# Kernel optimization log

Measured on AMD Instinct MI355X. Metric: run time of the kernel, lower is better.

Reference implementation:

```python
import jax, jax.numpy as jnp
import numpy as np

MODEL_DIM = 1024
NUM_HEADS = 16
HEAD_DIM = MODEL_DIM // NUM_HEADS
EPS = 1e-12
CHUNK = 128  # chunk size for the linear-attention recurrence


def setup_inputs() -> dict:
    key = jax.random.key(0)
    kx, kq, kk, kv, ko = jax.random.split(key, 5)
    b, l = 4, 4096
    x = jax.random.normal(kx, (b, l, MODEL_DIM), dtype=jnp.float32)
    # nn.Linear weights, init std=0.02, no bias; torch Linear computes x @ W.T
    Wq = 0.02 * jax.random.normal(kq, (MODEL_DIM, MODEL_DIM), dtype=jnp.float32)
    Wk = 0.02 * jax.random.normal(kk, (MODEL_DIM, MODEL_DIM), dtype=jnp.float32)
    Wv = 0.02 * jax.random.normal(kv, (MODEL_DIM, MODEL_DIM), dtype=jnp.float32)
    Wo = 0.02 * jax.random.normal(ko, (MODEL_DIM, MODEL_DIM), dtype=jnp.float32)
    return {"x": x, "Wq": Wq, "Wk": Wk, "Wv": Wv, "Wo": Wo}


def _pos_elu(t):
    # feature_map = F.elu(x) + 1
    return jax.nn.elu(t) + 1.0


def _linear_attention(q, k, v):
    # q,k,v: (b,h,l,d) with feature map already applied.
    # Causal linear attention: out_t = (q_t . sum_{s<=t} k_s v_s^T) / (q_t . sum_{s<=t} k_s) + EPS
    # Chunked recurrence over the (d,d) KV state avoids the (b,h,l,d,d) cumsum.
    b, h, l, d = q.shape
    nc = l // CHUNK
    qc = jnp.moveaxis(q.reshape(b, h, nc, CHUNK, d), 2, 0)  # (nc,b,h,C,d)
    kc = jnp.moveaxis(k.reshape(b, h, nc, CHUNK, d), 2, 0)
    vc = jnp.moveaxis(v.reshape(b, h, nc, CHUNK, d), 2, 0)
    mask = jnp.tril(jnp.ones((CHUNK, CHUNK), dtype=q.dtype))  # causal within chunk

    def step(carry, inp):
        S, z = carry  # S:(b,h,d,d) running sum k v^T; z:(b,h,d) running sum k
        qb, kb, vb = inp  # (b,h,C,d)
        scores = jnp.einsum('bhcd,bhsd->bhcs', qb, kb) * mask  # (b,h,C,C)
        num = jnp.einsum('bhcd,bhde->bhce', qb, S) + jnp.einsum('bhcs,bhse->bhce', scores, vb)
        den = jnp.einsum('bhcd,bhd->bhc', qb, z) + scores.sum(-1)  # (b,h,C)
        out = num / den[..., None] + EPS  # NOTE: eps added after division, as in source
        S = S + jnp.einsum('bhsd,bhse->bhde', kb, vb)
        z = z + kb.sum(axis=2)
        return (S, z), out

    S0 = jnp.zeros((b, h, d, d), dtype=q.dtype)
    z0 = jnp.zeros((b, h, d), dtype=q.dtype)
    _, outs = jax.lax.scan(step, (S0, z0), (qc, kc, vc))  # (nc,b,h,C,d)
    # -> (b, l, h, d)
    return jnp.moveaxis(outs, 0, 1).transpose(0, 3, 1, 2, 4).reshape(b, h * 0 + l // l, 0, 0) if False else outs


def reference(x, Wq, Wk, Wv, Wo):
    b, l, D = x.shape
    h, d = NUM_HEADS, HEAD_DIM
    # projections (torch Linear: x @ W.T), split heads -> (b,h,l,d)
    q = (x @ Wq.T).reshape(b, l, h, d).transpose(0, 2, 1, 3)
    k = (x @ Wk.T).reshape(b, l, h, d).transpose(0, 2, 1, 3)
    v = (x @ Wv.T).reshape(b, l, h, d).transpose(0, 2, 1, 3)
    q = _pos_elu(q)
    k = _pos_elu(k)
    outs = _linear_attention(q, k, v)  # (nc,b,h,C,d)
    nc = l // CHUNK
    # (nc,b,h,C,d) -> (b,nc,C,h,d) -> (b,l,D)  (matches transpose(1,2).view in torch)
    attn = outs.transpose(1, 0, 3, 2, 4).reshape(b, l, D)
    return attn @ Wo.T
```

## Files before the change

kernel.cpp:

```cpp
#include <hip/hip_runtime.h>
#include <stdint.h>

typedef float f32x4 __attribute__((ext_vector_type(4)));
typedef __bf16 bf16x8 __attribute__((ext_vector_type(8)));
typedef unsigned short u16x8 __attribute__((ext_vector_type(8)));

#define DEV __device__ __forceinline__

DEV unsigned short f2bf(float f) {
  unsigned int u = __float_as_uint(f);
  unsigned int r = (u + 0x7FFFu + ((u >> 16) & 1u)) >> 16;
  return (unsigned short)r;
}
DEV float b2f(unsigned short h) { return __uint_as_float(((unsigned int)h) << 16); }

DEV void gload16(const void* g, void* l) {
  __builtin_amdgcn_global_load_lds((__attribute__((address_space(1))) void*)(g),
                                   (__attribute__((address_space(3))) void*)(l), 16, 0, 0);
}

__global__ void cast_bf16_kernel(const float* __restrict__ in,
                                 unsigned short* __restrict__ out, int n8) {
  int i = blockIdx.x * 256 + threadIdx.x;
  if (i >= n8) return;
  const float4* p = (const float4*)in + (size_t)i * 2;
  float4 a = p[0], b = p[1];
  u16x8 o;
  o[0] = f2bf(a.x); o[1] = f2bf(a.y); o[2] = f2bf(a.z); o[3] = f2bf(a.w);
  o[4] = f2bf(b.x); o[5] = f2bf(b.y); o[6] = f2bf(b.z); o[7] = f2bf(b.w);
  ((u16x8*)out)[i] = o;
}

__global__ void cast_w4(const float* __restrict__ Wq, const float* __restrict__ Wk,
                        const float* __restrict__ Wv, const float* __restrict__ Wo,
                        unsigned short* __restrict__ wqkv, unsigned short* __restrict__ wo) {
  int i = blockIdx.x * 256 + threadIdx.x;
  int sel = i >> 17, j = i & 131071;
  const float* src = (sel == 0) ? Wq : (sel == 1) ? Wk : (sel == 2) ? Wv : Wo;
  unsigned short* dst = (sel < 3) ? (wqkv + (size_t)sel * 1048576) : wo;
  const float4* p = (const float4*)src + (size_t)j * 2;
  float4 a = p[0], b = p[1];
  u16x8 o;
  o[0] = f2bf(a.x); o[1] = f2bf(a.y); o[2] = f2bf(a.z); o[3] = f2bf(a.w);
  o[4] = f2bf(b.x); o[5] = f2bf(b.y); o[6] = f2bf(b.z); o[7] = f2bf(b.w);
  ((u16x8*)dst)[j] = o;
}

template<int MODE>
__global__ __launch_bounds__(256, 2) void gemm_bt(
    const unsigned short* __restrict__ A, const unsigned short* __restrict__ Bw,
    void* __restrict__ out0, unsigned short* __restrict__ qp,
    unsigned short* __restrict__ kp, unsigned short* __restrict__ vp,
    int K, int N, int nTn)
{
  __shared__ unsigned short sA[128 * 64];
  __shared__ unsigned short sB[128 * 64];
  int t = threadIdx.x, w = t >> 6, lane = t & 63, fr = lane & 15, fq = lane >> 4;
  int nwg = gridDim.x, cpx = nwg >> 3;
  int bid = (blockIdx.x & 7) * cpx + (blockIdx.x >> 3);
  int bm = bid / nTn, bn = bid % nTn;
  int wm = w >> 1, wn = w & 1;

  f32x4 acc[4][4];
  f32x4 z4 = {0.f, 0.f, 0.f, 0.f};
#pragma unroll
  for (int mi = 0; mi < 4; ++mi)
#pragma unroll
    for (int ni = 0; ni < 4; ++ni) acc[mi][ni] = z4;

  for (int k0 = 0; k0 < K; k0 += 64) {
#pragma unroll
    for (int i = 0; i < 4; ++i) {
      int p = (i * 4 + w) * 64 + lane;
      int r = p >> 3;
      int c8 = (p & 7) ^ (r & 7);
      gload16(A + (size_t)(bm * 128 + r) * K + k0 + c8 * 8, &sA[(i * 4 + w) * 512]);
      gload16(Bw + (size_t)(bn * 128 + r) * K + k0 + c8 * 8, &sB[(i * 4 + w) * 512]);
    }
    __syncthreads();
#pragma unroll
    for (int ks = 0; ks < 2; ++ks) {
      bf16x8 af[4], bg[4];
#pragma unroll
      for (int mi = 0; mi < 4; ++mi) {
        int r = wm * 64 + mi * 16 + fr;
        int c8 = (ks * 4 + fq) ^ (r & 7);
        af[mi] = *(const bf16x8*)&sA[(r * 8 + c8) * 8];
      }
#pragma unroll
      for (int ni = 0; ni < 4; ++ni) {
        int r = wn * 64 + ni * 16 + fr;
        int c8 = (ks * 4 + fq) ^ (r & 7);
        bg[ni] = *(const bf16x8*)&sB[(r * 8 + c8) * 8];
      }
#pragma unroll
      for (int mi = 0; mi < 4; ++mi)
#pragma unroll
        for (int ni = 0; ni < 4; ++ni)
          acc[mi][ni] = __builtin_amdgcn_mfma_f32_16x16x32_bf16(af[mi], bg[ni], acc[mi][ni], 0, 0, 0);
    }
    __syncthreads();
  }

  if (MODE == 0) {
    float* O = (float*)out0;
#pragma unroll
    for (int mi = 0; mi < 4; ++mi)
#pragma unroll
      for (int ni = 0; ni < 4; ++ni)
#pragma unroll
        for (int j = 0; j < 4; ++j) {
          int m = bm * 128 + wm * 64 + mi * 16 + fq * 4 + j;
          int n = bn * 128 + wn * 64 + ni * 16 + fr;
          O[(size_t)m * N + n] = acc[mi][ni][j];
        }
  } else {
    int tsel = (bn * 128) >> 10;
    unsigned short* base = (tsel == 0) ? qp : ((tsel == 1) ? kp : vp);
#pragma unroll
    for (int mi = 0; mi < 4; ++mi)
#pragma unroll
      for (int ni = 0; ni < 4; ++ni)
#pragma unroll
        for (int j = 0; j < 4; ++j) {
          int m = bm * 128 + wm * 64 + mi * 16 + fq * 4 + j;
          int n = bn * 128 + wn * 64 + ni * 16 + fr;
          int col1 = n & 1023;
          int h = col1 >> 6, d = col1 & 63;
          int b = m >> 12, l = m & 4095;
          float v = acc[mi][ni][j];
          if (tsel < 2) v = (v > 0.f) ? (v + 1.f) : __expf(v);
          base[(((size_t)(b * 16 + h)) * 4096 + l) * 64 + d] = f2bf(v);
        }
  }
}

__global__ __launch_bounds__(256) void chunk_state(
    const unsigned short* __restrict__ kb, const unsigned short* __restrict__ vb,
    float* __restrict__ Sbuf, float* __restrict__ zbuf)
{
  __shared__ unsigned short kT[64 * 136];
  __shared__ unsigned short vT[64 * 136];
  int t = threadIdx.x, w = t >> 6, lane = t & 63, fr = lane & 15, fq = lane >> 4;
  int bh = blockIdx.x >> 5, c = blockIdx.x & 31;
  size_t base = ((size_t)bh * 4096 + (size_t)c * 128) * 64;

  int s = t >> 1, d0 = (t & 1) * 32;
  const unsigned short* kpp = kb + base + (size_t)s * 64 + d0;
  const unsigned short* vpp = vb + base + (size_t)s * 64 + d0;
#pragma unroll
  for (int i = 0; i < 4; ++i) {
    u16x8 kr = *(const u16x8*)(kpp + i * 8);
    u16x8 vr = *(const u16x8*)(vpp + i * 8);
#pragma unroll
    for (int j = 0; j < 8; ++j) {
      int d = d0 + i * 8 + j;
      kT[d * 136 + s] = kr[j];
      vT[d * 136 + s] = vr[j];
    }
  }
  __syncthreads();

  f32x4 acc[4];
  f32x4 z4 = {0.f, 0.f, 0.f, 0.f};
#pragma unroll
  for (int n = 0; n < 4; ++n) acc[n] = z4;
#pragma unroll
  for (int ks = 0; ks < 4; ++ks) {
    bf16x8 av = *(const bf16x8*)&vT[(w * 16 + fr) * 136 + ks * 32 + fq * 8];
#pragma unroll
    for (int n = 0; n < 4; ++n) {
      bf16x8 bk = *(const bf16x8*)&kT[(n * 16 + fr) * 136 + ks * 32 + fq * 8];
      acc[n] = __builtin_amdgcn_mfma_f32_16x16x32_bf16(av, bk, acc[n], 0, 0, 0);
    }
  }
  size_t ob = ((size_t)bh * 32 + c) * 4096;
#pragma unroll
  for (int n = 0; n < 4; ++n)
#pragma unroll
    for (int j = 0; j < 4; ++j) {
      int e = w * 16 + fq * 4 + j, d = n * 16 + fr;
      Sbuf[ob + (size_t)e * 64 + d] = acc[n][j];
    }
  if (t < 64) {
    float z = 0.f;
#pragma unroll
    for (int i = 0; i < 16; ++i) {
      u16x8 kr = *(const u16x8*)&kT[t * 136 + i * 8];
#pragma unroll
      for (int j = 0; j < 8; ++j) z += b2f(kr[j]);
    }
    zbuf[((size_t)bh * 32 + c) * 64 + t] = z;
  }
}

__global__ __launch_bounds__(256) void scan_S(
    const float* __restrict__ Sbuf, unsigned short* __restrict__ Spref)
{
  int idx = blockIdx.x * 256 + threadIdx.x;
  int bh = idx >> 12, i = idx & 4095;
  size_t base = (size_t)bh * 32 * 4096 + i;
  float run = 0.f;
#pragma unroll
  for (int c = 0; c < 32; ++c) {
    float v = Sbuf[base + (size_t)c * 4096];
    Spref[base + (size_t)c * 4096] = f2bf(run);
    run += v;
  }
}

__global__ __launch_bounds__(256) void scan_z(
    const float* __restrict__ zbuf, float* __restrict__ zpref)
{
  int idx = blockIdx.x * 256 + threadIdx.x;
  size_t base = (size_t)(idx >> 6) * 32 * 64 + (idx & 63);
  float run = 0.f;
#pragma unroll
  for (int c = 0; c < 32; ++c) {
    float v = zbuf[base + c * 64];
    zpref[base + c * 64] = run;
    run += v;
  }
}

__global__ __launch_bounds__(256, 2) void chunk_out(
    const unsigned short* __restrict__ qb, const unsigned short* __restrict__ kb,
    const unsigned short* __restrict__ vb, const unsigned short* __restrict__ Spref,
    const float* __restrict__ zpref, unsigned short* __restrict__ attn)
{
  __shared__ unsigned short sq[128 * 64];
  __shared__ unsigned short skv[128 * 64];
  __shared__ unsigned short ss[128 * 128];
  __shared__ unsigned short sS[80 * 64];
  int t = threadIdx.x, w = t >> 6, lane = t & 63, fr = lane & 15, fq = lane >> 4;
  int bh = blockIdx.x >> 5, c = blockIdx.x & 31;
  size_t qkbase = ((size_t)bh * 4096 + (size_t)c * 128) * 64;
  size_t sbase = ((size_t)bh * 32 + c) * 4096;

  u16x8 vreg[4];
#pragma unroll
  for (int i = 0; i < 4; ++i)
    vreg[i] = *(const u16x8*)(vb + qkbase + (size_t)(t * 4 + i) * 8);

#pragma unroll
  for (int i = 0; i < 4; ++i) {
    int p = t * 4 + i, r = p >> 3, c8 = p & 7;
    int sw = (r * 8 + (c8 ^ (r & 7))) * 8;
    *(u16x8*)&sq[sw] = *(const u16x8*)(qb + qkbase + (size_t)p * 8);
    *(u16x8*)&skv[sw] = *(const u16x8*)(kb + qkbase + (size_t)p * 8);
  }
#pragma unroll
  for (int i = 0; i < 2; ++i) {
    int p = t * 2 + i, e = p >> 3, c8 = p & 7;
    *(u16x8*)&sS[(e * 8 + (c8 ^ (e & 7))) * 8] = *(const u16x8*)(Spref + sbase + (size_t)p * 8);
  }
  if (t < 64) sS[64 * 64 + t] = f2bf(zpref[((size_t)bh * 32 + c) * 64 + t]);
  {
    unsigned int* zz = (unsigned int*)&sS[65 * 64];
    for (int i = t; i < 480; i += 256) zz[i] = 0u;
  }
  __syncthreads();

  int rowbase = w * 32;
  bf16x8 aq[2][2];
#pragma unroll
  for (int mi = 0; mi < 2; ++mi)
#pragma unroll
    for (int kt = 0; kt < 2; ++kt) {
      int r = rowbase + mi * 16 + fr;
      int c8 = (kt * 4 + fq) ^ (r & 7);
      aq[mi][kt] = *(const bf16x8*)&sq[(r * 8 + c8) * 8];
    }

  f32x4 accs[2][8];
  f32x4 z4 = {0.f, 0.f, 0.f, 0.f};
#pragma unroll
  for (int mi = 0; mi < 2; ++mi)
#pragma unroll
    for (int ni = 0; ni < 8; ++ni) accs[mi][ni] = z4;

#pragma unroll
  for (int ni = 0; ni < 8; ++ni)
#pragma unroll
    for (int kt = 0; kt < 2; ++kt) {
      int r = ni * 16 + fr;
      int c8 = (kt * 4 + fq) ^ (r & 7);
      bf16x8 bk = *(const bf16x8*)&skv[(r * 8 + c8) * 8];
      accs[0][ni] = __builtin_amdgcn_mfma_f32_16x16x32_bf16(aq[0][kt], bk, accs[0][ni], 0, 0, 0);
      accs[1][ni] = __builtin_amdgcn_mfma_f32_16x16x32_bf16(aq[1][kt], bk, accs[1][ni], 0, 0, 0);
    }

  float rs[2][4];
#pragma unroll
  for (int mi = 0; mi < 2; ++mi)
#pragma unroll
    for (int j = 0; j < 4; ++j) {
      int srow = rowbase + mi * 16 + fq * 4 + j;
      float sum = 0.f;
#pragma unroll
      for (int ni = 0; ni < 8; ++ni) {
        int scol = ni * 16 + fr;
        float v = accs[mi][ni][j];
        v = (scol <= srow) ? v : 0.f;
        accs[mi][ni][j] = v;
        sum += v;
      }
#pragma unroll
      for (int msk = 1; msk < 16; msk <<= 1) sum += __shfl_xor(sum, msk, 64);
      rs[mi][j] = sum;
    }
  __syncthreads();

#pragma unroll
  for (int i = 0; i < 4; ++i) {
    int p = t * 4 + i, s = p >> 3, e0g = (p & 7) * 8;
#pragma unroll
    for (int j = 0; j < 8; ++j) {
      int e = e0g + j;
      skv[(e * 16 + ((s >> 3) ^ (e & 15))) * 8 + (s & 7)] = vreg[i][j];
    }
  }
#pragma unroll
  for (int mi = 0; mi < 2; ++mi)
#pragma unroll
    for (int ni = 0; ni < 8; ++ni)
#pragma unroll
      for (int j = 0; j < 4; ++j) {
        int srow = rowbase + mi * 16 + fq * 4 + j;
        int scol = ni * 16 + fr;
        ss[(srow * 16 + ((scol >> 3) ^ (srow & 15))) * 8 + (scol & 7)] = f2bf(accs[mi][ni][j]);
      }
  __syncthreads();

  f32x4 acco[2][4];
  f32x4 accd[2];
#pragma unroll
  for (int mi = 0; mi < 2; ++mi) {
    accd[mi] = z4;
#pragma unroll
    for (int ni = 0; ni < 4; ++ni) acco[mi][ni] = z4;
  }
#pragma unroll
  for (int kt = 0; kt < 2; ++kt) {
#pragma unroll
    for (int ni = 0; ni < 4; ++ni) {
      int r = ni * 16 + fr;
      int c8 = (kt * 4 + fq) ^ (r & 7);
      bf16x8 bS = *(const bf16x8*)&sS[(r * 8 + c8) * 8];
      acco[0][ni] = __builtin_amdgcn_mfma_f32_16x16x32_bf16(aq[0][kt], bS, acco[0][ni], 0, 0, 0);
      acco[1][ni] = __builtin_amdgcn_mfma_f32_16x16x32_bf16(aq[1][kt], bS, acco[1][ni], 0, 0, 0);
    }
    {
      int r = 64 + fr;
      int c8 = (kt * 4 + fq) ^ (r & 7);
      bf16x8 bz = *(const bf16x8*)&sS[(r * 8 + c8) * 8];
      accd[0] = __builtin_amdgcn_mfma_f32_16x16x32_bf16(aq[0][kt], bz, accd[0], 0, 0, 0);
      accd[1] = __builtin_amdgcn_mfma_f32_16x16x32_bf16(aq[1][kt], bz, accd[1], 0, 0, 0);
    }
  }
#pragma unroll
  for (int kt = 0; kt < 4; ++kt) {
    bf16x8 am[2];
#pragma unroll
    for (int mi = 0; mi < 2; ++mi) {
      int r = rowbase + mi * 16 + fr;
      int c8 = (kt * 4 + fq) ^ (r & 15);
      am[mi] = *(const bf16x8*)&ss[(r * 16 + c8) * 8];
    }
#pragma unroll
    for (int ni = 0; ni < 4; ++ni) {
      int r = ni * 16 + fr;
      int c8 = (kt * 4 + fq) ^ (r & 15);
      bf16x8 bv = *(const bf16x8*)&skv[(r * 16 + c8) * 8];
      acco[0][ni] = __builtin_amdgcn_mfma_f32_16x16x32_bf16(am[0], bv, acco[0][ni], 0, 0, 0);
      acco[1][ni] = __builtin_amdgcn_mfma_f32_16x16x32_bf16(am[1], bv, acco[1][ni], 0, 0, 0);
    }
  }

  int b = bh >> 4, h = bh & 15;
#pragma unroll
  for (int mi = 0; mi < 2; ++mi)
#pragma unroll
    for (int j = 0; j < 4; ++j) {
      float den = __shfl(accd[mi][j], (lane & 48), 64) + rs[mi][j];
      float rden = 1.f / den;
      int m = rowbase + mi * 16 + fq * 4 + j;
      size_t rowoff = ((size_t)b * 4096 + (size_t)c * 128 + m) * 1024 + h * 64;
#pragma unroll
      for (int ni = 0; ni < 4; ++ni) {
        int e = ni * 16 + fr;
        float o = acco[mi][ni][j] * rden + 1e-12f;
        attn[rowoff + e] = f2bf(o);
      }
    }
}

extern "C" void kernel_launch(void* const* d_in, const int* in_sizes, int n_in,
                              void* d_out, int out_size, void* d_ws, size_t ws_size,
                              hipStream_t stream) {
  (void)in_sizes; (void)n_in; (void)out_size; (void)ws_size;
  const float* x = (const float*)d_in[0];
  const float* Wq = (const float*)d_in[1];
  const float* Wk = (const float*)d_in[2];
  const float* Wv = (const float*)d_in[3];
  const float* Wo = (const float*)d_in[4];
  char* ws = (char*)d_ws;
  unsigned short* xbf  = (unsigned short*)(ws + 0);
  unsigned short* wqkv = (unsigned short*)(ws + 33554432);
  unsigned short* wo   = (unsigned short*)(ws + 39845888);
  unsigned short* q    = (unsigned short*)(ws + 41943040);
  unsigned short* k    = (unsigned short*)(ws + 75497472);
  unsigned short* v    = (unsigned short*)(ws + 109051904);
  unsigned short* attn = (unsigned short*)(ws + 142606336);
  float* Sbuf          = (float*)(ws + 176160768);
  unsigned short* Spref= (unsigned short*)(ws + 209715200);
  float* zbuf          = (float*)(ws + 226492416);
  float* zpref         = (float*)(ws + 227016704);

  cast_bf16_kernel<<<8192, 256, 0, stream>>>(x, xbf, 2097152);
  cast_w4<<<2048, 256, 0, stream>>>(Wq, Wk, Wv, Wo, wqkv, wo);

  gemm_bt<1><<<3072, 256, 0, stream>>>(xbf, wqkv, nullptr, q, k, v, 1024, 3072, 24);
  chunk_state<<<2048, 256, 0, stream>>>(k, v, Sbuf, zbuf);
  scan_S<<<1024, 256, 0, stream>>>(Sbuf, Spref);
  scan_z<<<16, 256, 0, stream>>>(zbuf, zpref);
  chunk_out<<<2048, 256, 0, stream>>>(q, k, v, Spref, zpref, attn);
  gemm_bt<0><<<1024, 256, 0, stream>>>(attn, wo, d_out, nullptr, nullptr, nullptr, 1024, 1024, 8);
}
```

Before: 234.8 us.

## Fuse x bf16 cast into QKV GEMM, merge scan kernels, drop block swizzle

Removes the standalone fp32->bf16 cast of x: the QKV GEMM now loads fp32 x through registers, converts it, and writes it to swizzled LDS, while B still uses direct global-to-LDS loads. The two prefix-scan kernels are merged into one launch, and the XCD-aware block remapping in the GEMM is replaced by plain blockIdx ordering. This saves a 64MB round trip and a kernel launch, but the A tile is now read at twice the bytes per GEMM tile with register staging and no async LDS path, which may stall the GEMM main loop. Dropping the swizzle may also hurt L2 locality across XCDs.

```diff
diff --git a/kernel.cpp b/kernel.cpp
--- a/kernel.cpp
+++ b/kernel.cpp
@@ -17,18 +17,6 @@
 DEV void gload16(const void* g, void* l) {
   __builtin_amdgcn_global_load_lds((__attribute__((address_space(1))) void*)(g),
                                    (__attribute__((address_space(3))) void*)(l), 16, 0, 0);
-}
-
-__global__ void cast_bf16_kernel(const float* __restrict__ in,
-                                 unsigned short* __restrict__ out, int n8) {
-  int i = blockIdx.x * 256 + threadIdx.x;
-  if (i >= n8) return;
-  const float4* p = (const float4*)in + (size_t)i * 2;
-  float4 a = p[0], b = p[1];
-  u16x8 o;
-  o[0] = f2bf(a.x); o[1] = f2bf(a.y); o[2] = f2bf(a.z); o[3] = f2bf(a.w);
-  o[4] = f2bf(b.x); o[5] = f2bf(b.y); o[6] = f2bf(b.z); o[7] = f2bf(b.w);
-  ((u16x8*)out)[i] = o;
 }
 
 __global__ void cast_w4(const float* __restrict__ Wq, const float* __restrict__ Wk,
@@ -48,7 +36,7 @@
 
 template<int MODE>
 __global__ __launch_bounds__(256, 2) void gemm_bt(
-    const unsigned short* __restrict__ A, const unsigned short* __restrict__ Bw,
+    const void* __restrict__ Aptr, const unsigned short* __restrict__ Bw,
     void* __restrict__ out0, unsigned short* __restrict__ qp,
     unsigned short* __restrict__ kp, unsigned short* __restrict__ vp,
     int K, int N, int nTn)
@@ -56,8 +44,7 @@
   __shared__ unsigned short sA[128 * 64];
   __shared__ unsigned short sB[128 * 64];
   int t = threadIdx.x, w = t >> 6, lane = t & 63, fr = lane & 15, fq = lane >> 4;
-  int nwg = gridDim.x, cpx = nwg >> 3;
-  int bid = (blockIdx.x & 7) * cpx + (blockIdx.x >> 3);
+  int bid = blockIdx.x;
   int bm = bid / nTn, bn = bid % nTn;
   int wm = w >> 1, wn = w & 1;
 
@@ -69,13 +56,45 @@
     for (int ni = 0; ni < 4; ++ni) acc[mi][ni] = z4;
 
   for (int k0 = 0; k0 < K; k0 += 64) {
-#pragma unroll
-    for (int i = 0; i < 4; ++i) {
-      int p = (i * 4 + w) * 64 + lane;
-      int r = p >> 3;
-      int c8 = (p & 7) ^ (r & 7);
-      gload16(A + (size_t)(bm * 128 + r) * K + k0 + c8 * 8, &sA[(i * 4 + w) * 512]);
-      gload16(Bw + (size_t)(bn * 128 + r) * K + k0 + c8 * 8, &sB[(i * 4 + w) * 512]);
+    if (MODE == 1) {
+      const float* A32 = (const float*)Aptr;
+#pragma unroll
+      for (int i = 0; i < 4; ++i) {
+        int p = (i * 4 + w) * 64 + lane;
+        int r = p >> 3;
+        int c8 = (p & 7) ^ (r & 7);
+        gload16(Bw + (size_t)(bn * 128 + r) * K + k0 + c8 * 8, &sB[(i * 4 + w) * 512]);
+      }
+      float4 av[4][2];
+#pragma unroll
+      for (int i = 0; i < 4; ++i) {
+        int p = (i * 4 + w) * 64 + lane;
+        int r = p >> 3, c8 = p & 7;
+        const float* s = A32 + (size_t)(bm * 128 + r) * K + k0 + c8 * 8;
+        av[i][0] = *(const float4*)s;
+        av[i][1] = *(const float4*)(s + 4);
+      }
+#pragma unroll
+      for (int i = 0; i < 4; ++i) {
+        int p = (i * 4 + w) * 64 + lane;
+        int r = p >> 3, c8 = p & 7;
+        u16x8 o;
+        o[0] = f2bf(av[i][0].x); o[1] = f2bf(av[i][0].y);
+        o[2] = f2bf(av[i][0].z); o[3] = f2bf(av[i][0].w);
+        o[4] = f2bf(av[i][1].x); o[5] = f2bf(av[i][1].y);
+        o[6] = f2bf(av[i][1].z); o[7] = f2bf(av[i][1].w);
+        *(u16x8*)&sA[(r * 8 + (c8 ^ (r & 7))) * 8] = o;
+      }
+    } else {
+      const unsigned short* A16 = (const unsigned short*)Aptr;
+#pragma unroll
+      for (int i = 0; i < 4; ++i) {
+        int p = (i * 4 + w) * 64 + lane;
+        int r = p >> 3;
+        int c8 = (p & 7) ^ (r & 7);
+        gload16(A16 + (size_t)(bm * 128 + r) * K + k0 + c8 * 8, &sA[(i * 4 + w) * 512]);
+        gload16(Bw + (size_t)(bn * 128 + r) * K + k0 + c8 * 8, &sB[(i * 4 + w) * 512]);
+      }
     }
     __syncthreads();
 #pragma unroll
@@ -194,32 +213,31 @@
   }
 }
 
-__global__ __launch_bounds__(256) void scan_S(
-    const float* __restrict__ Sbuf, unsigned short* __restrict__ Spref)
+__global__ __launch_bounds__(256) void scan_all(
+    const float* __restrict__ Sbuf, const float* __restrict__ zbuf,
+    unsigned short* __restrict__ Spref, float* __restrict__ zpref)
 {
-  int idx = blockIdx.x * 256 + threadIdx.x;
-  int bh = idx >> 12, i = idx & 4095;
-  size_t base = (size_t)bh * 32 * 4096 + i;
-  float run = 0.f;
-#pragma unroll
-  for (int c = 0; c < 32; ++c) {
-    float v = Sbuf[base + (size_t)c * 4096];
-    Spref[base + (size_t)c * 4096] = f2bf(run);
-    run += v;
-  }
-}
-
-__global__ __launch_bounds__(256) void scan_z(
-    const float* __restrict__ zbuf, float* __restrict__ zpref)
-{
-  int idx = blockIdx.x * 256 + threadIdx.x;
-  size_t base = (size_t)(idx >> 6) * 32 * 64 + (idx & 63);
-  float run = 0.f;
-#pragma unroll
-  for (int c = 0; c < 32; ++c) {
-    float v = zbuf[base + c * 64];
-    zpref[base + c * 64] = run;
-    run += v;
+  if (blockIdx.x < 1024) {
+    int idx = blockIdx.x * 256 + threadIdx.x;
+    int bh = idx >> 12, i = idx & 4095;
+    size_t base = (size_t)bh * 32 * 4096 + i;
+    float run = 0.f;
+#pragma unroll
+    for (int c = 0; c < 32; ++c) {
+      float v = Sbuf[base + (size_t)c * 4096];
+      Spref[base + (size_t)c * 4096] = f2bf(run);
+      run += v;
+    }
+  } else {
+    int idx = (blockIdx.x - 1024) * 256 + threadIdx.x;
+    size_t base = (size_t)(idx >> 6) * 32 * 64 + (idx & 63);
+    float run = 0.f;
+#pragma unroll
+    for (int c = 0; c < 32; ++c) {
+      float v = zbuf[base + c * 64];
+      zpref[base + c * 64] = run;
+      run += v;
+    }
   }
 }
 
@@ -405,7 +423,6 @@
   const float* Wv = (const float*)d_in[3];
   const float* Wo = (const float*)d_in[4];
   char* ws = (char*)d_ws;
-  unsigned short* xbf  = (unsigned short*)(ws + 0);
   unsigned short* wqkv = (unsigned short*)(ws + 33554432);
   unsigned short* wo   = (unsigned short*)(ws + 39845888);
   unsigned short* q    = (unsigned short*)(ws + 41943040);
@@ -417,13 +434,10 @@
   float* zbuf          = (float*)(ws + 226492416);
   float* zpref         = (float*)(ws + 227016704);
 
-  cast_bf16_kernel<<<8192, 256, 0, stream>>>(x, xbf, 2097152);
   cast_w4<<<2048, 256, 0, stream>>>(Wq, Wk, Wv, Wo, wqkv, wo);
-
-  gemm_bt<1><<<3072, 256, 0, stream>>>(xbf, wqkv, nullptr, q, k, v, 1024, 3072, 24);
+  gemm_bt<1><<<3072, 256, 0, stream>>>(x, wqkv, nullptr, q, k, v, 1024, 3072, 24);
   chunk_state<<<2048, 256, 0, stream>>>(k, v, Sbuf, zbuf);
-  scan_S<<<1024, 256, 0, stream>>>(Sbuf, Spref);
-  scan_z<<<16, 256, 0, stream>>>(zbuf, zpref);
+  scan_all<<<1040, 256, 0, stream>>>(Sbuf, zbuf, Spref, zpref);
   chunk_out<<<2048, 256, 0, stream>>>(q, k, v, Spref, zpref, attn);
   gemm_bt<0><<<1024, 256, 0, stream>>>(attn, wo, d_out, nullptr, nullptr, nullptr, 1024, 1024, 8);
 }
```

After: 288.2 us. 22.8% more time.
